# Kernel tuning notes

Measured on AMD Instinct MI355X. Metric: run time of the kernel, lower is better.

## Reference

```python
import jax, jax.numpy as jnp
import numpy as np

N_NODES = 50000
N_EDGES = 800000
IN_CH = 16
OUT_CH = 16
HID = 32


def setup_inputs() -> dict:
    key = jax.random.key(0)
    ks = jax.random.split(key, 10)
    features = jax.random.normal(ks[0], (N_NODES, IN_CH), dtype=jnp.float32)
    coords = jax.random.normal(ks[1], (N_NODES, 3), dtype=jnp.float32)
    # edges without self-loops (avoids zero-distance edges)
    row = jax.random.randint(ks[2], (N_EDGES,), 0, N_NODES, dtype=jnp.int32)
    off = jax.random.randint(ks[3], (N_EDGES,), 1, N_NODES, dtype=jnp.int32)
    col = (row + off) % N_NODES
    edge_index = jnp.stack([row, col], axis=0)
    # params (fan-in scaled like torch defaults, roughly)
    w1 = jax.random.normal(ks[4], (1, HID), dtype=jnp.float32)
    b1 = jnp.zeros((HID,), dtype=jnp.float32)
    w2 = jax.random.normal(ks[5], (HID, HID), dtype=jnp.float32) / np.sqrt(HID)
    b2 = jnp.zeros((HID,), dtype=jnp.float32)
    wc = jax.random.normal(ks[6], (HID, IN_CH * OUT_CH), dtype=jnp.float32) / np.sqrt(HID)
    bc = jnp.zeros((IN_CH * OUT_CH,), dtype=jnp.float32)
    return {"features": features, "coords": coords, "edge_index": edge_index,
            "w1": w1, "b1": b1, "w2": w2, "b2": b2, "wc": wc, "bc": bc}


def reference(features, coords, edge_index, w1, b1, w2, b2, wc, bc):
    row, col = edge_index[0], edge_index[1]
    rel_pos = coords[row] - coords[col]                      # [E, 3]
    distances = jnp.sqrt(jnp.sum(rel_pos * rel_pos, axis=-1, keepdims=True))  # [E, 1]
    h = jax.nn.silu(distances @ w1 + b1)                     # [E, H]
    h = jax.nn.silu(h @ w2 + b2)                             # [E, H]
    coeffs = (h @ wc + bc).reshape(-1, OUT_CH, IN_CH)        # [E, out, in]
    # Faithful to torch einsum 'noi,ei->no': the edge axes of coeffs and
    # neighbor_features are DISTINCT labels, so features[col] is summed over
    # all edges, then contracted with each edge's coeff matrix.
    feat_sum = jnp.sum(features[col], axis=0)                # [in]
    messages = jnp.einsum('eoi,i->eo', coeffs, feat_sum)     # [E, out]
    out = jnp.zeros((features.shape[0], OUT_CH), dtype=features.dtype)
    out = out.at[row].add(messages)                          # scatter-add
    return out
```

## Files before the change

kernel.cpp:

```cpp
#include <hip/hip_runtime.h>
#include <hip/hip_bf16.h>

#define IN_CH 16
#define OUT_CH 16
#define HID 32
#define NSLICE 4
#define SDEG 32
#define G_TAB 8192
#define DMAX 16.0f
#define RED_BLOCKS 64
#define TB 256
#define GB_BLOCKS 1024

__device__ __forceinline__ float silu(float x) {
  return x * __frcp_rn(1.f + __expf(-x));
}

__global__ __launch_bounds__(256) void k_zero(int4* __restrict__ p, int n4) {
  int i = blockIdx.x * blockDim.x + threadIdx.x;
  if (i < n4) p[i] = make_int4(0, 0, 0, 0);
}

__global__ __launch_bounds__(256) void k_pass1(
    const float* __restrict__ feat, const float* __restrict__ coords,
    const int* __restrict__ row, const int* __restrict__ col, int E, int N,
    int* __restrict__ cnt4, float* __restrict__ bucket,
    float* __restrict__ partials) {
  int e = blockIdx.x * blockDim.x + threadIdx.x;
  int lane = threadIdx.x & 63;
  int wave = threadIdx.x >> 6;
  bool act = (e < E);

  float s[IN_CH];
#pragma unroll
  for (int i = 0; i < IN_CH; ++i) s[i] = 0.f;

  int r = 0, pos = SDEG;
  float d = 0.f;
  int slice = blockIdx.x & (NSLICE - 1);

  if (act) {
    r = row[e];
    int c = col[e];

    float rx = coords[r * 3 + 0] - coords[c * 3 + 0];
    float ry = coords[r * 3 + 1] - coords[c * 3 + 1];
    float rz = coords[r * 3 + 2] - coords[c * 3 + 2];
    d = sqrtf(rx * rx + ry * ry + rz * rz);

    pos = atomicAdd(&cnt4[r * NSLICE + slice], 1);

    const float4* fp = reinterpret_cast<const float4*>(feat + (size_t)c * IN_CH);
    float4 a = fp[0], b = fp[1], cc = fp[2], dd = fp[3];
    s[0] = a.x;  s[1] = a.y;  s[2] = a.z;  s[3] = a.w;
    s[4] = b.x;  s[5] = b.y;  s[6] = b.z;  s[7] = b.w;
    s[8] = cc.x; s[9] = cc.y; s[10] = cc.z; s[11] = cc.w;
    s[12] = dd.x; s[13] = dd.y; s[14] = dd.z; s[15] = dd.w;
  }

  __shared__ float red[4][IN_CH];
#pragma unroll
  for (int i = 0; i < IN_CH; ++i) {
    float v = s[i];
#pragma unroll
    for (int off = 32; off > 0; off >>= 1) v += __shfl_down(v, off);
    s[i] = v;
  }
  if (lane == 0) {
#pragma unroll
    for (int i = 0; i < IN_CH; ++i) red[wave][i] = s[i];
  }
  __syncthreads();
  if (threadIdx.x < IN_CH) {
    int i = threadIdx.x;
    partials[(size_t)blockIdx.x * IN_CH + i] =
        red[0][i] + red[1][i] + red[2][i] + red[3][i];
  }

  if (act && pos < SDEG)
    bucket[((size_t)r * SDEG + pos) * NSLICE + slice] = d;
}

__global__ __launch_bounds__(256) void k_red(
    const float* __restrict__ partials, int nrows,
    const float* __restrict__ wc, const float* __restrict__ bc,
    float* __restrict__ stage2, int* __restrict__ done,
    float* __restrict__ wce, float* __restrict__ bce) {
  __shared__ float red[16][IN_CH];
  __shared__ float sfs[IN_CH];
  __shared__ int lastFlag;
  int t = threadIdx.x;
  int ch = t & 15, g = t >> 4;

  {
    int stream_id = blockIdx.x * 16 + g;
    int stride = 16 * RED_BLOCKS;
    float a = 0.f;
    for (int rr = stream_id; rr < nrows; rr += stride)
      a += partials[(size_t)rr * IN_CH + ch];
    red[g][ch] = a;
  }
  __syncthreads();
  if (t < IN_CH) {
    float s = 0.f;
#pragma unroll
    for (int g2 = 0; g2 < 16; ++g2) s += red[g2][t];
    stage2[blockIdx.x * IN_CH + t] = s;
  }
  __threadfence();
  __syncthreads();
  if (t == 0) lastFlag = (atomicAdd(done, 1) == RED_BLOCKS - 1);
  __syncthreads();
  if (!lastFlag) return;

  __threadfence();
  {
    int sg = t >> 4;
    float a = 0.f;
    for (int rr = sg; rr < RED_BLOCKS; rr += 16)
      a += stage2[rr * IN_CH + ch];
    red[sg][ch] = a;
  }
  __syncthreads();
  if (t < IN_CH) {
    float s = 0.f;
#pragma unroll
    for (int g2 = 0; g2 < 16; ++g2) s += red[g2][t];
    sfs[t] = s;
  }
  __syncthreads();

  for (int idx = t; idx < HID * OUT_CH; idx += 256) {
    int k = idx >> 4, o = idx & 15;
    float acc = 0.f;
#pragma unroll
    for (int i = 0; i < IN_CH; ++i)
      acc += wc[k * (IN_CH * OUT_CH) + o * IN_CH + i] * sfs[i];
    wce[idx] = acc;
  }
  if (t < OUT_CH) {
    float a = 0.f;
#pragma unroll
    for (int i = 0; i < IN_CH; ++i) a += bc[t * IN_CH + i] * sfs[i];
    bce[t] = a;
  }
}

__global__ __launch_bounds__(TB) void k_table(
    const float* __restrict__ w1, const float* __restrict__ b1,
    const float* __restrict__ w2, const float* __restrict__ b2,
    const float* __restrict__ wce, const float* __restrict__ bce,
    float* __restrict__ tableP) {
  __shared__ float F[TB][OUT_CH];
  int base = blockIdx.x * (TB - 1);
  int i = base + threadIdx.x;

  float m[OUT_CH];
#pragma unroll
  for (int o = 0; o < OUT_CH; ++o) m[o] = 0.f;

  if (i < G_TAB) {
    float d = (float)i * (DMAX / (float)(G_TAB - 1));

    float h1[HID];
#pragma unroll
    for (int k = 0; k < HID; ++k) h1[k] = silu(d * w1[k] + b1[k]);

    float h2[HID];
#pragma unroll
    for (int k = 0; k < HID; ++k) h2[k] = b2[k];
#pragma unroll
    for (int k = 0; k < HID; ++k) {
      float hk = h1[k];
#pragma unroll
      for (int j = 0; j < HID; ++j) h2[j] += hk * w2[k * HID + j];
    }

#pragma unroll
    for (int o = 0; o < OUT_CH; ++o) m[o] = bce[o];
#pragma unroll
    for (int k = 0; k < HID; ++k) {
      float hk = silu(h2[k]);
#pragma unroll
      for (int o = 0; o < OUT_CH; ++o) m[o] += hk * wce[k * OUT_CH + o];
    }
  }

#pragma unroll
  for (int o = 0; o < OUT_CH; ++o) F[threadIdx.x][o] = m[o];
  __syncthreads();

  const int NV4 = (TB - 1) * OUT_CH * 2 / 4;
  for (int v = threadIdx.x; v < NV4; v += TB) {
    int flat = v * 4;
    int p = flat >> 5;
    int w = flat & 31;
    int c0 = w >> 1;
    int P = base + p;
    if (P < G_TAB - 1) {
      float4 val = make_float4(F[p][c0], F[p + 1][c0],
                               F[p][c0 + 1], F[p + 1][c0 + 1]);
      *reinterpret_cast<float4*>(tableP + ((size_t)P * OUT_CH + c0) * 2) = val;
    }
  }
}

__global__ __launch_bounds__(256) void k_gather_tab(
    const int* __restrict__ cnt4, const float* __restrict__ bucket, int N,
    const float* __restrict__ tableP, float* __restrict__ out) {
  int wave = threadIdx.x >> 6;
  int lane = threadIdx.x & 63;
  int g = lane >> 4;
  int ch = lane & 15;
  const int nwaves = GB_BLOCKS * 4;

  int n = blockIdx.x * 4 + wave;
  if (n >= N) return;

  const float inv = (float)(G_TAB - 1) / DMAX;

  float dpre = bucket[(size_t)n * (SDEG * NSLICE) + lane];
  int cpre = (lane < NSLICE) ? cnt4[n * NSLICE + lane] : 0;

  while (true) {
    float dcur = dpre;
    int ccur = cpre;
    int nn = n + nwaves;
    if (nn < N) {
      dpre = bucket[(size_t)nn * (SDEG * NSLICE) + lane];
      cpre = (lane < NSLICE) ? cnt4[nn * NSLICE + lane] : 0;
    }

    int c0 = min(__shfl(ccur, 0), SDEG);
    int c1 = min(__shfl(ccur, 1), SDEG);
    int c2 = min(__shfl(ccur, 2), SDEG);
    int c3 = min(__shfl(ccur, 3), SDEG);
    int cntG = (g == 0) ? c0 : (g == 1) ? c1 : (g == 2) ? c2 : c3;
    int jmax = max(max(c0, c1), max(c2, c3));

    const float* nb = bucket + (size_t)n * (SDEG * NSLICE);
    float acc = 0.f;
    for (int j = 0; j < jmax; j += 2) {
      float da = __shfl(dcur, j * NSLICE + g);
      float db = __shfl(dcur, (j + 1) * NSLICE + g);
      if (j >= 16) da = nb[j * NSLICE + g];
      if (j + 1 >= 16) db = nb[(j + 1) * NSLICE + g];
      bool pa = (j < cntG), pb = (j + 1 < cntG);

      float xa = da * inv;
      int ia = (int)xa;
      ia = ia < 0 ? 0 : (ia > G_TAB - 2 ? G_TAB - 2 : ia);
      float fa = xa - (float)ia;
      float xb = db * inv;
      int ib = (int)xb;
      ib = ib < 0 ? 0 : (ib > G_TAB - 2 ? G_TAB - 2 : ib);
      float fb = xb - (float)ib;

      if (pa) {
        float2 F = *reinterpret_cast<const float2*>(
            tableP + ((size_t)ia * OUT_CH + ch) * 2);
        acc += F.x + fa * (F.y - F.x);
      }
      if (pb) {
        float2 F = *reinterpret_cast<const float2*>(
            tableP + ((size_t)ib * OUT_CH + ch) * 2);
        acc += F.x + fb * (F.y - F.x);
      }
    }

    acc += __shfl_xor(acc, 16);
    acc += __shfl_xor(acc, 32);
    if (lane < OUT_CH) out[(size_t)n * OUT_CH + lane] = acc;

    if (nn >= N) break;
    n = nn;
  }
}

__global__ __launch_bounds__(512) void k_wce_fb(
    const float* __restrict__ rows_in, int nrows,
    const float* __restrict__ wc, const float* __restrict__ bc,
    float* __restrict__ wce, float* __restrict__ bce) {
  __shared__ float seg[32][IN_CH];
  __shared__ float sfs[IN_CH];
  int t = threadIdx.x;
  {
    int ch = t & 15, sg = t >> 4;
    float a = 0.f;
    for (int rr = sg; rr < nrows; rr += 32)
      a += rows_in[(size_t)rr * IN_CH + ch];
    seg[sg][ch] = a;
  }
  __syncthreads();
  if (t < IN_CH) {
    float a = 0.f;
#pragma unroll
    for (int sg = 0; sg < 32; ++sg) a += seg[sg][t];
    sfs[t] = a;
  }
  __syncthreads();
  int k = t >> 4, o = t & 15;
  float acc = 0.f;
#pragma unroll
  for (int i = 0; i < IN_CH; ++i)
    acc += wc[k * (IN_CH * OUT_CH) + o * IN_CH + i] * sfs[i];
  wce[t] = acc;
  if (t < OUT_CH) {
    float a = 0.f;
#pragma unroll
    for (int i = 0; i < IN_CH; ++i) a += bc[t * IN_CH + i] * sfs[i];
    bce[t] = a;
  }
}

__global__ __launch_bounds__(256) void k_hist(
    const int* __restrict__ col, int E, int* __restrict__ ccnt) {
  int e = blockIdx.x * blockDim.x + threadIdx.x;
  if (e < E) atomicAdd(&ccnt[col[e]], 1);
}

__global__ __launch_bounds__(256) void k_fs(
    const float* __restrict__ feat, const int* __restrict__ ccnt, int N,
    float* __restrict__ partials) {
  int ch = threadIdx.x & 15;
  int slot = threadIdx.x >> 4;
  int gs = blockIdx.x * 16 + slot;
  int stride = 16 * gridDim.x;
  float a = 0.f;
  for (int n = gs; n < N; n += stride)
    a += (float)ccnt[n] * feat[(size_t)n * IN_CH + ch];
  __shared__ float red[16][IN_CH];
  red[slot][ch] = a;
  __syncthreads();
  if (threadIdx.x < IN_CH) {
    int i = threadIdx.x;
    float s = 0.f;
#pragma unroll
    for (int g = 0; g < 16; ++g) s += red[g][i];
    partials[(size_t)blockIdx.x * IN_CH + i] = s;
  }
}

__global__ __launch_bounds__(256) void k_edges_atomic(
    const float* __restrict__ coords, const int* __restrict__ row,
    const int* __restrict__ col, int E,
    const float* __restrict__ w1, const float* __restrict__ b1,
    const float* __restrict__ w2, const float* __restrict__ b2,
    const float* __restrict__ wce, const float* __restrict__ bce,
    float* __restrict__ out) {
  int e = blockIdx.x * blockDim.x + threadIdx.x;
  if (e >= E) return;
  int r = row[e], c = col[e];
  float rx = coords[r * 3 + 0] - coords[c * 3 + 0];
  float ry = coords[r * 3 + 1] - coords[c * 3 + 1];
  float rz = coords[r * 3 + 2] - coords[c * 3 + 2];
  float d = sqrtf(rx * rx + ry * ry + rz * rz);
  float h1[HID];
#pragma unroll
  for (int k = 0; k < HID; ++k) h1[k] = silu(d * w1[k] + b1[k]);
  float h2[HID];
#pragma unroll
  for (int k = 0; k < HID; ++k) h2[k] = b2[k];
#pragma unroll
  for (int k = 0; k < HID; ++k) {
    float hk = h1[k];
#pragma unroll
    for (int j = 0; j < HID; ++j) h2[j] += hk * w2[k * HID + j];
  }
  float m[OUT_CH];
#pragma unroll
  for (int o = 0; o < OUT_CH; ++o) m[o] = bce[o];
#pragma unroll
  for (int k = 0; k < HID; ++k) {
    float hk = silu(h2[k]);
#pragma unroll
    for (int o = 0; o < OUT_CH; ++o) m[o] += hk * wce[k * OUT_CH + o];
  }
  float* op = out + (size_t)r * OUT_CH;
#pragma unroll
  for (int o = 0; o < OUT_CH; ++o) atomicAdd(op + o, m[o]);
}

extern "C" void kernel_launch(void* const* d_in, const int* in_sizes, int n_in,
                              void* d_out, int out_size, void* d_ws,
                              size_t ws_size, hipStream_t stream) {
  const float* features = (const float*)d_in[0];
  const float* coords   = (const float*)d_in[1];
  const int*   eidx     = (const int*)d_in[2];
  const float* w1       = (const float*)d_in[3];
  const float* b1       = (const float*)d_in[4];
  const float* w2       = (const float*)d_in[5];
  const float* b2       = (const float*)d_in[6];
  const float* wc       = (const float*)d_in[7];
  const float* bc       = (const float*)d_in[8];

  const int E = in_sizes[2] / 2;
  const int N = in_sizes[0] / IN_CH;
  const int* row = eidx;
  const int* col = eidx + E;

  float* out = (float*)d_out;
  float* ws  = (float*)d_ws;
  const int eb = (E + 255) / 256;

  size_t off = 0;
  float* wce = ws + off;      off += 512;
  float* bce = ws + off;      off += 16;
  float* stage2 = ws + off;   off += RED_BLOCKS * IN_CH;
  float* partials = ws + off; off += (size_t)eb * IN_CH;
  off = (off + 63) & ~(size_t)63;
  float* tableP = ws + off;   off += (size_t)G_TAB * OUT_CH * 2;
  off = (off + 63) & ~(size_t)63;
  int* done = (int*)(ws + off);   off += 16;
  int* cnt4 = (int*)(ws + off);   off += (size_t)N * NSLICE;
  off = (off + 63) & ~(size_t)63;
  float* bucket = ws + off;       off += (size_t)N * NSLICE * SDEG;
  size_t needed = off * 4;

  if (ws_size >= needed) {
    int n4 = (int)((16 + (size_t)N * NSLICE) / 4);
    k_zero<<<(n4 + 255) / 256, 256, 0, stream>>>((int4*)done, n4);
    k_pass1<<<eb, 256, 0, stream>>>(features, coords, row, col, E, N, cnt4,
                                    bucket, partials);
    k_red<<<RED_BLOCKS, 256, 0, stream>>>(partials, eb, wc, bc, stage2, done,
                                          wce, bce);
    int tb_grid = (G_TAB - 1 + (TB - 1) - 1) / (TB - 1) + 1;
    k_table<<<tb_grid, TB, 0, stream>>>(w1, b1, w2, b2, wce, bce, tableP);
    int gb = min(GB_BLOCKS, (N + 3) / 4);
    k_gather_tab<<<gb, 256, 0, stream>>>(cnt4, bucket, N, tableP, out);
  } else {
    float* partials_fb = bce + 16;
    int*   ccnt_fb     = (int*)(partials_fb + 64 * IN_CH);
    int nz4 = (N + 3) / 4;
    k_zero<<<(nz4 + 255) / 256, 256, 0, stream>>>((int4*)ccnt_fb, nz4);
    hipMemsetAsync(out, 0, (size_t)out_size * sizeof(float), stream);
    k_hist<<<(E + 255) / 256, 256, 0, stream>>>(col, E, ccnt_fb);
    k_fs<<<64, 256, 0, stream>>>(features, ccnt_fb, N, partials_fb);
    k_wce_fb<<<1, 512, 0, stream>>>(partials_fb, 64, wc, bc, wce, bce);
    k_edges_atomic<<<(E + 255) / 256, 256, 0, stream>>>(coords, row, col, E,
                                                        w1, b1, w2, b2, wce,
                                                        bce, out);
  }
}
```

Measured before the change: 110.6 us.

## Shrink lookup table and stage it in LDS for gather interpolation

```diff
diff --git a/kernel.cpp b/kernel.cpp
--- a/kernel.cpp
+++ b/kernel.cpp
@@ -6,11 +6,10 @@
 #define HID 32
 #define NSLICE 4
 #define SDEG 32
-#define G_TAB 8192
+#define G_TAB 1024
 #define DMAX 16.0f
 #define RED_BLOCKS 64
-#define TB 256
-#define GB_BLOCKS 1024
+#define GB_BLOCKS 512
 
 __device__ __forceinline__ float silu(float x) {
   return x * __frcp_rn(1.f + __expf(-x));
@@ -146,68 +145,57 @@
   }
 }
 
-__global__ __launch_bounds__(TB) void k_table(
+__global__ __launch_bounds__(256) void k_table(
     const float* __restrict__ w1, const float* __restrict__ b1,
     const float* __restrict__ w2, const float* __restrict__ b2,
     const float* __restrict__ wce, const float* __restrict__ bce,
-    float* __restrict__ tableP) {
-  __shared__ float F[TB][OUT_CH];
-  int base = blockIdx.x * (TB - 1);
-  int i = base + threadIdx.x;
+    float* __restrict__ table) {
+  int i = blockIdx.x * blockDim.x + threadIdx.x;
+  if (i >= G_TAB) return;
+  float d = (float)i * (DMAX / (float)(G_TAB - 1));
+
+  float h1[HID];
+#pragma unroll
+  for (int k = 0; k < HID; ++k) h1[k] = silu(d * w1[k] + b1[k]);
+
+  float h2[HID];
+#pragma unroll
+  for (int k = 0; k < HID; ++k) h2[k] = b2[k];
+#pragma unroll
+  for (int k = 0; k < HID; ++k) {
+    float hk = h1[k];
+#pragma unroll
+    for (int j = 0; j < HID; ++j) h2[j] += hk * w2[k * HID + j];
+  }
 
   float m[OUT_CH];
 #pragma unroll
-  for (int o = 0; o < OUT_CH; ++o) m[o] = 0.f;
-
-  if (i < G_TAB) {
-    float d = (float)i * (DMAX / (float)(G_TAB - 1));
-
-    float h1[HID];
-#pragma unroll
-    for (int k = 0; k < HID; ++k) h1[k] = silu(d * w1[k] + b1[k]);
-
-    float h2[HID];
-#pragma unroll
-    for (int k = 0; k < HID; ++k) h2[k] = b2[k];
-#pragma unroll
-    for (int k = 0; k < HID; ++k) {
-      float hk = h1[k];
-#pragma unroll
-      for (int j = 0; j < HID; ++j) h2[j] += hk * w2[k * HID + j];
-    }
-
-#pragma unroll
-    for (int o = 0; o < OUT_CH; ++o) m[o] = bce[o];
-#pragma unroll
-    for (int k = 0; k < HID; ++k) {
-      float hk = silu(h2[k]);
-#pragma unroll
-      for (int o = 0; o < OUT_CH; ++o) m[o] += hk * wce[k * OUT_CH + o];
-    }
-  }
-
-#pragma unroll
-  for (int o = 0; o < OUT_CH; ++o) F[threadIdx.x][o] = m[o];
-  __syncthreads();
-
-  const int NV4 = (TB - 1) * OUT_CH * 2 / 4;
-  for (int v = threadIdx.x; v < NV4; v += TB) {
-    int flat = v * 4;
-    int p = flat >> 5;
-    int w = flat & 31;
-    int c0 = w >> 1;
-    int P = base + p;
-    if (P < G_TAB - 1) {
-      float4 val = make_float4(F[p][c0], F[p + 1][c0],
-                               F[p][c0 + 1], F[p + 1][c0 + 1]);
-      *reinterpret_cast<float4*>(tableP + ((size_t)P * OUT_CH + c0) * 2) = val;
-    }
-  }
+  for (int o = 0; o < OUT_CH; ++o) m[o] = bce[o];
+#pragma unroll
+  for (int k = 0; k < HID; ++k) {
+    float hk = silu(h2[k]);
+#pragma unroll
+    for (int o = 0; o < OUT_CH; ++o) m[o] += hk * wce[k * OUT_CH + o];
+  }
+
+  float4* tp = reinterpret_cast<float4*>(table + (size_t)i * OUT_CH);
+  tp[0] = make_float4(m[0], m[1], m[2], m[3]);
+  tp[1] = make_float4(m[4], m[5], m[6], m[7]);
+  tp[2] = make_float4(m[8], m[9], m[10], m[11]);
+  tp[3] = make_float4(m[12], m[13], m[14], m[15]);
 }
 
 __global__ __launch_bounds__(256) void k_gather_tab(
     const int* __restrict__ cnt4, const float* __restrict__ bucket, int N,
-    const float* __restrict__ tableP, float* __restrict__ out) {
+    const float* __restrict__ tableG, float* __restrict__ out) {
+  __shared__ float tab[G_TAB][OUT_CH];
+  {
+    const float4* src = reinterpret_cast<const float4*>(tableG);
+    float4* dst = reinterpret_cast<float4*>(&tab[0][0]);
+    for (int v = threadIdx.x; v < G_TAB * OUT_CH / 4; v += 256) dst[v] = src[v];
+  }
+  __syncthreads();
+
   int wave = threadIdx.x >> 6;
   int lane = threadIdx.x & 63;
   int g = lane >> 4;
@@ -257,14 +245,12 @@
       float fb = xb - (float)ib;
 
       if (pa) {
-        float2 F = *reinterpret_cast<const float2*>(
-            tableP + ((size_t)ia * OUT_CH + ch) * 2);
-        acc += F.x + fa * (F.y - F.x);
+        float f0 = tab[ia][ch], f1 = tab[ia + 1][ch];
+        acc += f0 + fa * (f1 - f0);
       }
       if (pb) {
-        float2 F = *reinterpret_cast<const float2*>(
-            tableP + ((size_t)ib * OUT_CH + ch) * 2);
-        acc += F.x + fb * (F.y - F.x);
+        float f0 = tab[ib][ch], f1 = tab[ib + 1][ch];
+        acc += f0 + fb * (f1 - f0);
       }
     }
 
@@ -409,7 +395,7 @@
   float* stage2 = ws + off;   off += RED_BLOCKS * IN_CH;
   float* partials = ws + off; off += (size_t)eb * IN_CH;
   off = (off + 63) & ~(size_t)63;
-  float* tableP = ws + off;   off += (size_t)G_TAB * OUT_CH * 2;
+  float* table = ws + off;    off += (size_t)G_TAB * OUT_CH;
   off = (off + 63) & ~(size_t)63;
   int* done = (int*)(ws + off);   off += 16;
   int* cnt4 = (int*)(ws + off);   off += (size_t)N * NSLICE;
@@ -424,10 +410,10 @@
                                     bucket, partials);
     k_red<<<RED_BLOCKS, 256, 0, stream>>>(partials, eb, wc, bc, stage2, done,
                                           wce, bce);
-    int tb_grid = (G_TAB - 1 + (TB - 1) - 1) / (TB - 1) + 1;
-    k_table<<<tb_grid, TB, 0, stream>>>(w1, b1, w2, b2, wce, bce, tableP);
+    k_table<<<(G_TAB + 255) / 256, 256, 0, stream>>>(w1, b1, w2, b2, wce, bce,
+                                                     table);
     int gb = min(GB_BLOCKS, (N + 3) / 4);
-    k_gather_tab<<<gb, 256, 0, stream>>>(cnt4, bucket, N, tableP, out);
+    k_gather_tab<<<gb, 256, 0, stream>>>(cnt4, bucket, N, table, out);
   } else {
     float* partials_fb = bce + 16;
     int*   ccnt_fb     = (int*)(partials_fb + 64 * IN_CH);
```

New measurement: 111.5 us. No clear change (+0.8%).
